# Kernel optimization log

Hardware: AMD Instinct MI355X
Metric: run time of the kernel (lower is better)

## Reference

```python
import jax, jax.numpy as jnp
import numpy as np

B, C, H, W = 64, 1, 256, 256        # x shape; seq_len = C*H = 256, input_dim = W = 256
E, HID, L, NCLS = 512, 1024, 2, 10


def _lstm_layer(xs, h0, c0, Wx, bx, Wh, bh):
    """xs: [S,B,in] -> ys: [S,B,HID]. Gate order: f, i, g(candidate), o."""
    def step(carry, xt):
        h, c = carry
        gates = xt @ Wx + bx + h @ Wh + bh            # [B, 4*HID] (fuses 8 tiny Linears into 2 GEMMs)
        f, i, g, o = jnp.split(gates, 4, axis=-1)
        f = jax.nn.sigmoid(f)
        i = jax.nn.sigmoid(i)
        g = jnp.tanh(g)
        o = jax.nn.sigmoid(o)
        c = f * c + i * g
        h = o * jnp.tanh(c)
        return (h, c), h
    (hT, cT), ys = jax.lax.scan(step, (h0, c0), xs)
    return ys


def setup_inputs() -> dict:
    key = jax.random.key(0)
    ks = jax.random.split(key, 16)
    s = 0.02
    inp = {
        "x": jax.random.normal(ks[0], (B, C, H, W), jnp.float32),
        "h0": jax.random.normal(ks[1], (L, B, HID), jnp.float32),
        "c0": jax.random.normal(ks[2], (L, B, HID), jnp.float32),
        "W_enc": jax.random.normal(ks[3], (W, E), jnp.float32) * s,
        "b_enc": jnp.zeros((E,), jnp.float32),
        "alpha": jnp.float32(0.25),  # PReLU default single-parameter weight
        "Wx0": jax.random.normal(ks[4], (E, 4 * HID), jnp.float32) * s,
        "bx0": jnp.zeros((4 * HID,), jnp.float32),
        "Wh0": jax.random.normal(ks[5], (HID, 4 * HID), jnp.float32) * s,
        "bh0": jnp.zeros((4 * HID,), jnp.float32),
        "Wx1": jax.random.normal(ks[6], (HID, 4 * HID), jnp.float32) * s,
        "bx1": jnp.zeros((4 * HID,), jnp.float32),
        "Wh1": jax.random.normal(ks[7], (HID, 4 * HID), jnp.float32) * s,
        "bh1": jnp.zeros((4 * HID,), jnp.float32),
        "W_cls": jax.random.normal(ks[8], (HID, NCLS), jnp.float32) * s,
        "b_cls": jnp.zeros((NCLS,), jnp.float32),
    }
    return inp


def reference(x, h0, c0, W_enc, b_enc, alpha, Wx0, bx0, Wh0, bh0,
              Wx1, bx1, Wh1, bh1, W_cls, b_cls):
    b, c, h, w = x.shape
    x = x.reshape(b, c * h, w)                    # [B, S, input_dim]
    e = x @ W_enc + b_enc                         # encoder Linear
    e = jnp.where(e >= 0, e, alpha * e)           # PReLU (single shared alpha)
    xs = jnp.swapaxes(e, 0, 1)                    # [S, B, E] for scan
    ys = _lstm_layer(xs, h0[0], c0[0], Wx0, bx0, Wh0, bh0)
    ys = _lstm_layer(ys, h0[1], c0[1], Wx1, bx1, Wh1, bh1)
    return ys[-1] @ W_cls + b_cls                 # classify last timestep -> [B, 10]
```

## Files before the change

kernel.cpp:

```cpp
#include <hip/hip_runtime.h>
#include <hip/hip_bf16.h>
#include <cstddef>


using short8 = __attribute__((ext_vector_type(8))) short;
using f32x4  = __attribute__((ext_vector_type(4))) float;

#define LD8(p) (*reinterpret_cast<const short8*>(p))

__device__ __forceinline__ float sigmoidf_(float x) {
    return 1.f / (1.f + __expf(-x));
}
__device__ __forceinline__ unsigned short f2bf(float x) {
    union { float f; unsigned u; } v; v.f = x;
    unsigned r = v.u + 0x7fffu + ((v.u >> 16) & 1u);
    return (unsigned short)(r >> 16);
}
__device__ __forceinline__ float bf2f(unsigned short h) {
    union { unsigned u; float f; } v; v.u = ((unsigned)h) << 16;
    return v.f;
}

__global__ __launch_bounds__(256) void enc_gemm_k(
    const float* __restrict__ A, const float* __restrict__ B,
    unsigned short* __restrict__ Ef,
    const float* __restrict__ bias1, const float* __restrict__ alphap,
    int M, int N, int K, int sB, int sS)
{
    __shared__ float As[128][17];
    __shared__ float Bs[16][64];
    const int tid = threadIdx.x;
    const int tx = tid & 15, ty = tid >> 4;
    const int rb = blockIdx.y * 128;
    const int cb = blockIdx.x * 64;

    float acc[8][4];
#pragma unroll
    for (int i = 0; i < 8; ++i)
#pragma unroll
        for (int j = 0; j < 4; ++j) acc[i][j] = 0.f;

    const int nk = K >> 4;
    for (int kt = 0; kt < nk; ++kt) {
        const int k0 = kt << 4;
        __syncthreads();
        {
            const int row = tid >> 2, k4 = tid & 3;
#pragma unroll
            for (int h = 0; h < 2; ++h) {
                const int r = rb + row + h * 64;
                const float4 v = *reinterpret_cast<const float4*>(
                    &A[(size_t)(r & 63) * sB + (size_t)(r >> 6) * sS + k0 + k4 * 4]);
                As[row + h * 64][k4 * 4 + 0] = v.x;
                As[row + h * 64][k4 * 4 + 1] = v.y;
                As[row + h * 64][k4 * 4 + 2] = v.z;
                As[row + h * 64][k4 * 4 + 3] = v.w;
            }
        }
        {
            const int bk = tid >> 4, c4 = tid & 15;
            *reinterpret_cast<float4*>(&Bs[bk][c4 * 4]) =
                *reinterpret_cast<const float4*>(
                    &B[(size_t)(k0 + bk) * N + cb + c4 * 4]);
        }
        __syncthreads();
#pragma unroll
        for (int k = 0; k < 16; ++k) {
            float a[8];
#pragma unroll
            for (int i = 0; i < 8; ++i) a[i] = As[ty * 8 + i][k];
            const float4 bv = *reinterpret_cast<const float4*>(&Bs[k][tx * 4]);
#pragma unroll
            for (int i = 0; i < 8; ++i) {
                acc[i][0] = fmaf(a[i], bv.x, acc[i][0]);
                acc[i][1] = fmaf(a[i], bv.y, acc[i][1]);
                acc[i][2] = fmaf(a[i], bv.z, acc[i][2]);
                acc[i][3] = fmaf(a[i], bv.w, acc[i][3]);
            }
        }
    }

    float bsum[4];
#pragma unroll
    for (int j = 0; j < 4; ++j) bsum[j] = bias1[cb + tx * 4 + j];
    const float alpha = alphap[0];
    const int k0c = cb + tx * 4;
    const int s = k0c >> 5, kg = (k0c >> 3) & 3, e0 = k0c & 7;
#pragma unroll
    for (int i = 0; i < 8; ++i) {
        const int r = rb + ty * 8 + i;
        const int t = r >> 6, b = r & 63;
        const int ln = (b & 15) + 16 * kg, nj = b >> 4;
        unsigned short hs[4], ls[4];
#pragma unroll
        for (int j = 0; j < 4; ++j) {
            float v = acc[i][j] + bsum[j];
            v = (v >= 0.f) ? v : alpha * v;
            hs[j] = f2bf(v);
            ls[j] = f2bf(v - bf2f(hs[j]));
        }
        uint2 hp, lp;
        hp.x = (unsigned)hs[0] | ((unsigned)hs[1] << 16);
        hp.y = (unsigned)hs[2] | ((unsigned)hs[3] << 16);
        lp.x = (unsigned)ls[0] | ((unsigned)ls[1] << 16);
        lp.y = (unsigned)ls[2] | ((unsigned)ls[3] << 16);
        const size_t base =
            ((((size_t)t * 32 + s) * 4 + nj) * 64 + ln) * 8 + e0;
        *reinterpret_cast<uint2*>(Ef + base) = hp;
        *reinterpret_cast<uint2*>(Ef + base + 32768) = lp;
    }
}

__global__ __launch_bounds__(256) void wprep_k(
    const float* __restrict__ Wa, const float* __restrict__ Wb,
    unsigned short* __restrict__ Wf, int NS)
{
    __shared__ float tl[32][65];
    const int k0 = blockIdx.x * 32, j0 = blockIdx.y * 64;
    const int tid = threadIdx.x;
    {
        const int kk = tid >> 3, jq = tid & 7;
        const int k = k0 + kk;
        const float* src = (k < 1024) ? &Wa[(size_t)k * 4096]
                                      : &Wb[(size_t)(k - 1024) * 4096];
#pragma unroll
        for (int h = 0; h < 2; ++h) {
            const float4 v = *reinterpret_cast<const float4*>(
                &src[j0 + jq * 8 + h * 4]);
            tl[kk][jq * 8 + h * 4 + 0] = v.x; tl[kk][jq * 8 + h * 4 + 1] = v.y;
            tl[kk][jq * 8 + h * 4 + 2] = v.z; tl[kk][jq * 8 + h * 4 + 3] = v.w;
        }
    }
    __syncthreads();
    const int j = tid >> 2, kg = tid & 3;
    const int jg = j0 + j;
    const int g = jg >> 10, cc = jg & 1023;
    const int lb = cc >> 3, c = cc & 7;
    const int rloc = g * 8 + c;
    const int mi = rloc >> 4, r16 = rloc & 15;
    const int lane = r16 + 16 * kg;
    const int s = k0 >> 5;
    short8 hv, lv;
#pragma unroll
    for (int e = 0; e < 8; ++e) {
        const float x = tl[kg * 8 + e][j];
        const unsigned short h = f2bf(x);
        hv[e] = (short)h;
        lv[e] = (short)f2bf(x - bf2f(h));
    }
    const size_t oH = ((((size_t)lb * 2 + 0) * NS + s) * 2 + mi) * 512 + (size_t)lane * 8;
    const size_t oL = ((((size_t)lb * 2 + 1) * NS + s) * 2 + mi) * 512 + (size_t)lane * 8;
    *reinterpret_cast<short8*>(Wf + oH) = hv;
    *reinterpret_cast<short8*>(Wf + oL) = lv;
}

__global__ __launch_bounds__(256) void hsplit_k(
    const float* __restrict__ hrow, unsigned short* __restrict__ dst)
{
    const int idx = blockIdx.x * 256 + threadIdx.x;
    const int b = idx >> 7, gc = idx & 127;
    const int k = gc * 8;
    short8 hv, lv;
#pragma unroll
    for (int e = 0; e < 8; ++e) {
        const float x = hrow[(size_t)b * 1024 + k + e];
        const unsigned short h = f2bf(x);
        hv[e] = (short)h;
        lv[e] = (short)f2bf(x - bf2f(h));
    }
    const int s = k >> 5, kg = (k >> 3) & 3, nj = b >> 4;
    const int l = (b & 15) + 16 * kg;
    const size_t oH = (((size_t)(0 * 32 + s) * 4 + nj) * 64 + l) * 8;
    const size_t oL = (((size_t)(1 * 32 + s) * 4 + nj) * 64 + l) * 8;
    *reinterpret_cast<short8*>(dst + oH) = hv;
    *reinterpret_cast<short8*>(dst + oL) = lv;
}

__global__ __launch_bounds__(256) void bsum_k(
    const float* __restrict__ bx, const float* __restrict__ bh,
    float* __restrict__ out)
{
    const int r = blockIdx.x * 256 + threadIdx.x;
    const int lb = r >> 5, rl = r & 31;
    const int g = rl >> 3, c = rl & 7;
    const int j = g * 1024 + lb * 8 + c;
    out[r] = bx[j] + bh[j];
}

__global__ __launch_bounds__(512, 2) void fused_lstm_k(
    const unsigned short* __restrict__ Ef,
    const unsigned short* __restrict__ Wf0,
    const unsigned short* __restrict__ Wf1,
    unsigned short* __restrict__ Y0, unsigned short* __restrict__ H1,
    const float* __restrict__ c0, const float* __restrict__ bsum0p,
    const float* __restrict__ bsum1p, float* __restrict__ hst1,
    unsigned* bar)
{
    __shared__ float Pred[8][32][66];
    __shared__ unsigned short hasmH[64][8];
    __shared__ unsigned short hasmL[64][8];

    const int tid = threadIdx.x;
    const int lane = tid & 63;
    const int w = tid >> 6;
    const int bid = blockIdx.x;
    const int layer = bid >> 7;
    const int lb = bid & 127;

    const int NS = layer ? 64 : 48;
    const int nsub = layer ? 8 : 6;
    const int sub0 = w * nsub;
    const int wNS = NS * 1024;

    const unsigned short* Wf = layer ? Wf1 : Wf0;
    const unsigned short* wB =
        Wf + (size_t)lb * 2 * NS * 1024 + (size_t)lane * 8;

    short8 w00r[8], w01r[8], w10r[8], w11r[8];
#pragma unroll
    for (int s = 0; s < 8; ++s)
        if (s < nsub) {
            const unsigned short* wp = wB + (size_t)(sub0 + s) * 1024;
            w00r[s] = LD8(wp);        w01r[s] = LD8(wp + 512);
            w10r[s] = LD8(wp + wNS);  w11r[s] = LD8(wp + wNS + 512);
        }

    const int col = w;
    float c_ = c0[(size_t)layer * 65536 + (size_t)lane * 1024 + lb * 8 + col];
    const float* bsB = layer ? bsum1p : bsum0p;
    float bs[4];
#pragma unroll
    for (int g = 0; g < 4; ++g) bs[g] = bsB[lb * 32 + g * 8 + col];

    for (int r = 1; r <= 257; ++r) {
        const bool act = layer ? (r >= 2) : (r <= 256);
        if (act) {
            const int t = layer ? r - 2 : r - 1;
            const unsigned short* hOwn =
                (layer ? H1 : Y0) + (size_t)t * 131072 + (size_t)lane * 8;
            const unsigned short* hCross = layer
                ? Y0 + (size_t)(t + 1) * 131072 + (size_t)lane * 8
                : Ef + (size_t)t * 65536 + (size_t)lane * 8;
            const int poCross = layer ? 65536 : 32768;

            f32x4 acc[2][4] = {};
#pragma unroll
            for (int s = 0; s < 8; ++s)
                if (s < nsub) {
                    const int sg = sub0 + s;
                    const unsigned short* hp;
                    int po;
                    if (sg < 32) {
                        hp = hOwn + (size_t)sg * 2048;
                        po = 65536;
                    } else {
                        hp = hCross + (size_t)(sg - 32) * 2048;
                        po = poCross;
                    }
                    const short8 h0v = LD8(hp),        h1v = LD8(hp + 512);
                    const short8 h2v = LD8(hp + 1024), h3v = LD8(hp + 1536);
                    const short8 l0v = LD8(hp + po),        l1v = LD8(hp + po + 512);
                    const short8 l2v = LD8(hp + po + 1024), l3v = LD8(hp + po + 1536);
#define MM(mi, nj, HH, HL)                                                     \
    acc[mi][nj] = __builtin_amdgcn_mfma_f32_16x16x32_bf16(                     \
        (mi) ? w01r[s] : w00r[s], HH, acc[mi][nj], 0, 0, 0);                   \
    acc[mi][nj] = __builtin_amdgcn_mfma_f32_16x16x32_bf16(                     \
        (mi) ? w01r[s] : w00r[s], HL, acc[mi][nj], 0, 0, 0);                   \
    acc[mi][nj] = __builtin_amdgcn_mfma_f32_16x16x32_bf16(                     \
        (mi) ? w11r[s] : w10r[s], HH, acc[mi][nj], 0, 0, 0);
                    MM(0, 0, h0v, l0v)  MM(0, 1, h1v, l1v)
                    MM(0, 2, h2v, l2v)  MM(0, 3, h3v, l3v)
                    MM(1, 0, h0v, l0v)  MM(1, 1, h1v, l1v)
                    MM(1, 2, h2v, l2v)  MM(1, 3, h3v, l3v)
#undef MM
                }

            {
                const int rq = (lane >> 4) * 4, cq = lane & 15;
#pragma unroll
                for (int mi = 0; mi < 2; ++mi)
#pragma unroll
                    for (int nj = 0; nj < 4; ++nj)
#pragma unroll
                        for (int rr = 0; rr < 4; ++rr)
                            Pred[w][mi * 16 + rq + rr][nj * 16 + cq] =
                                acc[mi][nj][rr];
            }
            __syncthreads();

            {
                float p[4];
#pragma unroll
                for (int g = 0; g < 4; ++g) {
                    const int row = g * 8 + col;
                    float s0 = 0.f;
#pragma unroll
                    for (int ww = 0; ww < 8; ++ww)
                        s0 += Pred[ww][row][lane];
                    p[g] = s0 + bs[g];
                }
                const float fg = sigmoidf_(p[0]);
                const float ig = sigmoidf_(p[1]);
                const float gg = tanhf(p[2]);
                const float og = sigmoidf_(p[3]);
                c_ = fmaf(fg, c_, ig * gg);
                const float h = og * tanhf(c_);
                const unsigned short hh = f2bf(h);
                hasmH[lane][col] = hh;
                hasmL[lane][col] = f2bf(h - bf2f(hh));
                if (layer && r == 257)
                    hst1[(size_t)(lb * 8 + col) * 64 + lane] = h;
            }
            __syncthreads();

            if (tid < 128) {
                const int p = tid >> 6, b = tid & 63;
                unsigned short* hw =
                    (layer ? H1 : Y0) + (size_t)(t + 1) * 131072;
                const size_t off =
                    (((size_t)(p * 32 + (lb >> 2)) * 4 + (b >> 4)) * 64 +
                     ((b & 15) + 16 * (lb & 3))) * 8;
                const unsigned long long* src =
                    reinterpret_cast<const unsigned long long*>(
                        p ? &hasmL[b][0] : &hasmH[b][0]);
                unsigned long long* dst =
                    reinterpret_cast<unsigned long long*>(hw + off);
                __hip_atomic_store(dst, src[0], __ATOMIC_RELAXED,
                                   __HIP_MEMORY_SCOPE_AGENT);
                __hip_atomic_store(dst + 1, src[1], __ATOMIC_RELAXED,
                                   __HIP_MEMORY_SCOPE_AGENT);
            }
        }

        if (r < 257) {
            __syncthreads();
            const unsigned rr = (unsigned)r;
            if (tid == 0)
                __hip_atomic_store(bar + (size_t)bid * 32, rr,
                                   __ATOMIC_RELAXED, __HIP_MEMORY_SCOPE_AGENT);
            if (bid == 0) {
                if (tid < 128) {
                    while (__hip_atomic_load(bar + (size_t)tid * 32,
                                             __ATOMIC_RELAXED,
                                             __HIP_MEMORY_SCOPE_AGENT) < rr)
                        __builtin_amdgcn_s_sleep(1);
                }
                __syncthreads();
                if (tid == 0)
#pragma unroll
                    for (int g = 0; g < 8; ++g)
                        __hip_atomic_store(bar + 8192 + g * 32, rr,
                                           __ATOMIC_RELAXED,
                                           __HIP_MEMORY_SCOPE_AGENT);
            } else if (bid == 128) {
                if (tid < 128) {
                    while (__hip_atomic_load(bar + (size_t)(128 + tid) * 32,
                                             __ATOMIC_RELAXED,
                                             __HIP_MEMORY_SCOPE_AGENT) < rr)
                        __builtin_amdgcn_s_sleep(1);
                }
                __syncthreads();
                if (tid == 0)
#pragma unroll
                    for (int g = 0; g < 8; ++g)
                        __hip_atomic_store(bar + 8704 + g * 32, rr,
                                           __ATOMIC_RELAXED,
                                           __HIP_MEMORY_SCOPE_AGENT);
            }
            if (tid == 0) {
                unsigned* g0 = bar + 8192 + (bid & 7) * 32;
                if (layer == 0) {
                    while (__hip_atomic_load(g0, __ATOMIC_RELAXED,
                                             __HIP_MEMORY_SCOPE_AGENT) < rr)
                        __builtin_amdgcn_s_sleep(1);
                } else {
                    unsigned* g1 = bar + 8704 + (bid & 7) * 32;
                    for (;;) {
                        const unsigned a = __hip_atomic_load(
                            g1, __ATOMIC_RELAXED, __HIP_MEMORY_SCOPE_AGENT);
                        const unsigned b = __hip_atomic_load(
                            g0, __ATOMIC_RELAXED, __HIP_MEMORY_SCOPE_AGENT);
                        if (a >= rr && b >= rr) break;
                        __builtin_amdgcn_s_sleep(1);
                    }
                }
                __builtin_amdgcn_fence(__ATOMIC_ACQUIRE, "agent");
            }
            __syncthreads();
        }
    }
}

__global__ __launch_bounds__(256) void cls_k(
    const float* __restrict__ hfin, const float* __restrict__ Wc,
    const float* __restrict__ bcls, float* __restrict__ out)
{
    __shared__ float red[4][64];
    const int n = blockIdx.x;
    const int lane = threadIdx.x & 63, w = threadIdx.x >> 6;
    float acc = 0.f;
    for (int k = w * 256; k < w * 256 + 256; ++k)
        acc = fmaf(hfin[k * 64 + lane], Wc[k * 10 + n], acc);
    red[w][lane] = acc;
    __syncthreads();
    if (w == 0) {
        out[lane * 10 + n] = red[0][lane] + red[1][lane] + red[2][lane] +
                             red[3][lane] + bcls[n];
    }
}

extern "C" void kernel_launch(void* const* d_in, const int* in_sizes, int n_in,
                              void* d_out, int out_size, void* d_ws,
                              size_t ws_size, hipStream_t stream)
{
    const float* x    = (const float*)d_in[0];
    const float* h0   = (const float*)d_in[1];
    const float* c0   = (const float*)d_in[2];
    const float* Wenc = (const float*)d_in[3];
    const float* benc = (const float*)d_in[4];
    const float* alpha= (const float*)d_in[5];
    const float* Wx0  = (const float*)d_in[6];
    const float* bx0  = (const float*)d_in[7];
    const float* Wh0  = (const float*)d_in[8];
    const float* bh0  = (const float*)d_in[9];
    const float* Wx1  = (const float*)d_in[10];
    const float* bx1  = (const float*)d_in[11];
    const float* Wh1  = (const float*)d_in[12];
    const float* bh1  = (const float*)d_in[13];
    const float* Wcls = (const float*)d_in[14];
    const float* bcls = (const float*)d_in[15];
    float* out = (float*)d_out;

    float* ws = (float*)d_ws;
    size_t off = 0;
    unsigned short* Ef   = (unsigned short*)(ws + off); off += 8388608;
    unsigned short* Wf0  = (unsigned short*)(ws + off); off += 6291456;
    unsigned short* Wf1  = (unsigned short*)(ws + off); off += 8388608;
    unsigned short* Y0   = (unsigned short*)(ws + off); off += 16842752;
    unsigned short* H1   = (unsigned short*)(ws + off); off += 16842752;
    float* bsum0p = ws + off; off += 4096;
    float* bsum1p = ws + off; off += 4096;
    float* hst1   = ws + off; off += 65536;
    unsigned* bars = (unsigned*)(ws + off); off += 16384;

    (void)hipMemsetAsync(bars, 0, 65536, stream);

    enc_gemm_k<<<dim3(8, 128), 256, 0, stream>>>(
        x, Wenc, Ef, benc, alpha, 16384, 512, 256, 65536, 256);
    wprep_k<<<dim3(48, 64), 256, 0, stream>>>(Wh0, Wx0, Wf0, 48);
    wprep_k<<<dim3(64, 64), 256, 0, stream>>>(Wh1, Wx1, Wf1, 64);
    hsplit_k<<<32, 256, 0, stream>>>(h0, Y0);
    hsplit_k<<<32, 256, 0, stream>>>(h0 + 65536, H1);
    bsum_k<<<16, 256, 0, stream>>>(bx0, bh0, bsum0p);
    bsum_k<<<16, 256, 0, stream>>>(bx1, bh1, bsum1p);

    fused_lstm_k<<<256, 512, 0, stream>>>(Ef, Wf0, Wf1, Y0, H1, c0,
                                          bsum0p, bsum1p, hst1, bars);

    cls_k<<<dim3(10), 256, 0, stream>>>(hst1, Wcls, bcls, out);
}
```

Measured before the change: 2.337 ms.

## Replace centralized grid barrier with direct flag polling and overlap input GEMM

The old per-step barrier had two hops: an aggregator block collected every block's flag, then broadcast a release flag. This is replaced by each block polling the 128 producer flags it actually depends on. Each wave now takes 4 recurrent subtiles plus 2 or 4 input subtiles, and it computes the input-side MFMAs before waiting on the recurrent h dependency. That hides part of the wait behind useful work and removes the serialized aggregation from the per-timestep critical path. The explicit acquire fence after the wait is gone, and the flag stores have no release fence, so memory-ordering correctness depends on relaxed atomics plus cache behaviour.

```diff
diff --git a/kernel.cpp b/kernel.cpp
--- a/kernel.cpp
+++ b/kernel.cpp
@@ -187,6 +187,17 @@
     out[r] = bx[j] + bh[j];
 }
 
+__device__ __forceinline__ void poll_flags(unsigned* bar, int base,
+                                           unsigned need, int tid) {
+    if (tid < 128) {
+        unsigned* p = bar + (size_t)(base + tid) * 32;
+        while (__hip_atomic_load(p, __ATOMIC_RELAXED,
+                                 __HIP_MEMORY_SCOPE_AGENT) < need)
+            __builtin_amdgcn_s_sleep(1);
+    }
+    __syncthreads();
+}
+
 __global__ __launch_bounds__(512, 2) void fused_lstm_k(
     const unsigned short* __restrict__ Ef,
     const unsigned short* __restrict__ Wf0,
@@ -208,8 +219,7 @@
     const int lb = bid & 127;
 
     const int NS = layer ? 64 : 48;
-    const int nsub = layer ? 8 : 6;
-    const int sub0 = w * nsub;
+    const int nEx = layer ? 4 : 2;
     const int wNS = NS * 1024;
 
     const unsigned short* Wf = layer ? Wf1 : Wf0;
@@ -218,11 +228,14 @@
 
     short8 w00r[8], w01r[8], w10r[8], w11r[8];
 #pragma unroll
-    for (int s = 0; s < 8; ++s)
-        if (s < nsub) {
-            const unsigned short* wp = wB + (size_t)(sub0 + s) * 1024;
-            w00r[s] = LD8(wp);        w01r[s] = LD8(wp + 512);
-            w10r[s] = LD8(wp + wNS);  w11r[s] = LD8(wp + wNS + 512);
+    for (int i = 0; i < 8; ++i)
+        if (i < 4 + nEx) {
+            const int sg = (i < 4)
+                ? (w * 4 + i)
+                : (layer ? (32 + w * 4 + (i - 4)) : (32 + w * 2 + (i - 4)));
+            const unsigned short* wp = wB + (size_t)sg * 1024;
+            w00r[i] = LD8(wp);        w01r[i] = LD8(wp + 512);
+            w10r[i] = LD8(wp + wNS);  w11r[i] = LD8(wp + wNS + 512);
         }
 
     const int col = w;
@@ -231,6 +244,25 @@
     float bs[4];
 #pragma unroll
     for (int g = 0; g < 4; ++g) bs[g] = bsB[lb * 32 + g * 8 + col];
+
+#define MM(mi, nj, HH, HL)                                                     \
+    acc[mi][nj] = __builtin_amdgcn_mfma_f32_16x16x32_bf16(                     \
+        (mi) ? w01r[i] : w00r[i], HH, acc[mi][nj], 0, 0, 0);                   \
+    acc[mi][nj] = __builtin_amdgcn_mfma_f32_16x16x32_bf16(                     \
+        (mi) ? w01r[i] : w00r[i], HL, acc[mi][nj], 0, 0, 0);                   \
+    acc[mi][nj] = __builtin_amdgcn_mfma_f32_16x16x32_bf16(                     \
+        (mi) ? w11r[i] : w10r[i], HH, acc[mi][nj], 0, 0, 0);
+#define SUBTILE(hp, po)                                                        \
+    {                                                                          \
+        const short8 h0v = LD8(hp),        h1v = LD8(hp + 512);                \
+        const short8 h2v = LD8(hp + 1024), h3v = LD8(hp + 1536);               \
+        const short8 l0v = LD8(hp + po),        l1v = LD8(hp + po + 512);      \
+        const short8 l2v = LD8(hp + po + 1024), l3v = LD8(hp + po + 1536);     \
+        MM(0, 0, h0v, l0v)  MM(0, 1, h1v, l1v)                                 \
+        MM(0, 2, h2v, l2v)  MM(0, 3, h3v, l3v)                                 \
+        MM(1, 0, h0v, l0v)  MM(1, 1, h1v, l1v)                                 \
+        MM(1, 2, h2v, l2v)  MM(1, 3, h3v, l3v)                                 \
+    }
 
     for (int r = 1; r <= 257; ++r) {
         const bool act = layer ? (r >= 2) : (r <= 256);
@@ -244,36 +276,22 @@
             const int poCross = layer ? 65536 : 32768;
 
             f32x4 acc[2][4] = {};
-#pragma unroll
-            for (int s = 0; s < 8; ++s)
-                if (s < nsub) {
-                    const int sg = sub0 + s;
-                    const unsigned short* hp;
-                    int po;
-                    if (sg < 32) {
-                        hp = hOwn + (size_t)sg * 2048;
-                        po = 65536;
-                    } else {
-                        hp = hCross + (size_t)(sg - 32) * 2048;
-                        po = poCross;
-                    }
-                    const short8 h0v = LD8(hp),        h1v = LD8(hp + 512);
-                    const short8 h2v = LD8(hp + 1024), h3v = LD8(hp + 1536);
-                    const short8 l0v = LD8(hp + po),        l1v = LD8(hp + po + 512);
-                    const short8 l2v = LD8(hp + po + 1024), l3v = LD8(hp + po + 1536);
-#define MM(mi, nj, HH, HL)                                                     \
-    acc[mi][nj] = __builtin_amdgcn_mfma_f32_16x16x32_bf16(                     \
-        (mi) ? w01r[s] : w00r[s], HH, acc[mi][nj], 0, 0, 0);                   \
-    acc[mi][nj] = __builtin_amdgcn_mfma_f32_16x16x32_bf16(                     \
-        (mi) ? w01r[s] : w00r[s], HL, acc[mi][nj], 0, 0, 0);                   \
-    acc[mi][nj] = __builtin_amdgcn_mfma_f32_16x16x32_bf16(                     \
-        (mi) ? w11r[s] : w10r[s], HH, acc[mi][nj], 0, 0, 0);
-                    MM(0, 0, h0v, l0v)  MM(0, 1, h1v, l1v)
-                    MM(0, 2, h2v, l2v)  MM(0, 3, h3v, l3v)
-                    MM(1, 0, h0v, l0v)  MM(1, 1, h1v, l1v)
-                    MM(1, 2, h2v, l2v)  MM(1, 3, h3v, l3v)
-#undef MM
+
+            if (layer) poll_flags(bar, 0, (unsigned)(r - 1), tid);
+#pragma unroll
+            for (int i = 4; i < 8; ++i)
+                if (i < 4 + nEx) {
+                    const int cs = layer ? (w * 4 + (i - 4)) : (w * 2 + (i - 4));
+                    const unsigned short* hp = hCross + (size_t)cs * 2048;
+                    SUBTILE(hp, poCross)
                 }
+
+            if (r >= 2) poll_flags(bar, layer ? 128 : 0, (unsigned)(r - 1), tid);
+#pragma unroll
+            for (int i = 0; i < 4; ++i) {
+                const unsigned short* hp = hOwn + (size_t)(w * 4 + i) * 2048;
+                SUBTILE(hp, 65536)
+            }
 
             {
                 const int rq = (lane >> 4) * 4, cq = lane & 15;
@@ -332,63 +350,15 @@
             }
         }
 
-        if (r < 257) {
+        if (r <= 256) {
             __syncthreads();
-            const unsigned rr = (unsigned)r;
             if (tid == 0)
-                __hip_atomic_store(bar + (size_t)bid * 32, rr,
+                __hip_atomic_store(bar + (size_t)bid * 32, (unsigned)r,
                                    __ATOMIC_RELAXED, __HIP_MEMORY_SCOPE_AGENT);
-            if (bid == 0) {
-                if (tid < 128) {
-                    while (__hip_atomic_load(bar + (size_t)tid * 32,
-                                             __ATOMIC_RELAXED,
-                                             __HIP_MEMORY_SCOPE_AGENT) < rr)
-                        __builtin_amdgcn_s_sleep(1);
-                }
-                __syncthreads();
-                if (tid == 0)
-#pragma unroll
-                    for (int g = 0; g < 8; ++g)
-                        __hip_atomic_store(bar + 8192 + g * 32, rr,
-                                           __ATOMIC_RELAXED,
-                                           __HIP_MEMORY_SCOPE_AGENT);
-            } else if (bid == 128) {
-                if (tid < 128) {
-                    while (__hip_atomic_load(bar + (size_t)(128 + tid) * 32,
-                                             __ATOMIC_RELAXED,
-                                             __HIP_MEMORY_SCOPE_AGENT) < rr)
-                        __builtin_amdgcn_s_sleep(1);
-                }
-                __syncthreads();
-                if (tid == 0)
-#pragma unroll
-                    for (int g = 0; g < 8; ++g)
-                        __hip_atomic_store(bar + 8704 + g * 32, rr,
-                                           __ATOMIC_RELAXED,
-                                           __HIP_MEMORY_SCOPE_AGENT);
-            }
-            if (tid == 0) {
-                unsigned* g0 = bar + 8192 + (bid & 7) * 32;
-                if (layer == 0) {
-                    while (__hip_atomic_load(g0, __ATOMIC_RELAXED,
-                                             __HIP_MEMORY_SCOPE_AGENT) < rr)
-                        __builtin_amdgcn_s_sleep(1);
-                } else {
-                    unsigned* g1 = bar + 8704 + (bid & 7) * 32;
-                    for (;;) {
-                        const unsigned a = __hip_atomic_load(
-                            g1, __ATOMIC_RELAXED, __HIP_MEMORY_SCOPE_AGENT);
-                        const unsigned b = __hip_atomic_load(
-                            g0, __ATOMIC_RELAXED, __HIP_MEMORY_SCOPE_AGENT);
-                        if (a >= rr && b >= rr) break;
-                        __builtin_amdgcn_s_sleep(1);
-                    }
-                }
-                __builtin_amdgcn_fence(__ATOMIC_ACQUIRE, "agent");
-            }
-            __syncthreads();
-        }
-    }
+        }
+    }
+#undef SUBTILE
+#undef MM
 }
 
 __global__ __launch_bounds__(256) void cls_k(
@@ -441,9 +411,9 @@
     float* bsum0p = ws + off; off += 4096;
     float* bsum1p = ws + off; off += 4096;
     float* hst1   = ws + off; off += 65536;
-    unsigned* bars = (unsigned*)(ws + off); off += 16384;
-
-    (void)hipMemsetAsync(bars, 0, 65536, stream);
+    unsigned* bars = (unsigned*)(ws + off); off += 8192;
+
+    (void)hipMemsetAsync(bars, 0, 32768, stream);
 
     enc_gemm_k<<<dim3(8, 128), 256, 0, stream>>>(
         x, Wenc, Ef, benc, alpha, 16384, 512, 256, 65536, 256);
```

Measured after the change: 1.913 ms. 1.22x faster.
